# Performance work log

Hardware: AMD Instinct MI355X
Metric: run time of the kernel (lower is better)

The kernel has to match this reference:

```python
import jax, jax.numpy as jnp
import numpy as np

B, CH, CW, H, FH, FW = 32, 16, 16, 8, 4, 4
NQ = 64
NK = CH * FH * CW * FW  # 4096
D_IN, D_V, D_MODEL = 512, 64, 512


def setup_inputs() -> dict:
    key = jax.random.key(0)
    k1, k2, k3, k4, k5 = jax.random.split(key, 5)
    att12 = jax.random.uniform(k1, (B, CH, CW, H, FH, FW), dtype=jnp.float32)
    att3 = jax.random.uniform(k2, (B, H, NQ, CH * CW), dtype=jnp.float32)
    values = jax.random.normal(k3, (B, NK, D_IN), dtype=jnp.float32)
    # Learned params (xavier-ish scale)
    W_v = jax.random.normal(k4, (H * D_V, D_IN), dtype=jnp.float32) * (1.0 / np.sqrt(D_IN))
    b_v = jnp.zeros((H * D_V,), dtype=jnp.float32)
    W_o = jax.random.normal(k5, (D_MODEL, H * D_V), dtype=jnp.float32) * (1.0 / np.sqrt(H * D_V))
    b_o = jnp.zeros((D_MODEL,), dtype=jnp.float32)
    return {"att12": att12, "att3": att3, "values": values,
            "W_v": W_v, "b_v": b_v, "W_o": W_o, "b_o": b_o}


def reference(att12, att3, values, W_v, b_v, W_o, b_o):
    b_s, h, nq, _ = att3.shape
    ch = cw = CH
    fh, fw = att12.shape[-2:]
    nk = values.shape[1]
    d_v = W_v.shape[0] // h
    # v: [b, h, nk, d_v]
    v = (values @ W_v.T + b_v).reshape(b_s, nk, h, d_v).transpose(0, 2, 1, 3)
    # att12 -> [b, h, 1, ch, cw, fh, fw]
    a12 = jnp.transpose(att12, (0, 3, 1, 2, 4, 5))[:, :, None]
    # att3 -> [b, h, nq, ch, cw, 1, 1]
    a3 = att3.reshape(b_s, h, nq, ch, cw, 1, 1)
    # broadcast multiply, then interleave to key order (ch, fh, cw, fw)
    att = (a12 * a3).transpose(0, 1, 2, 3, 5, 4, 6).reshape(b_s, h, nq, nk)
    att = jax.nn.softmax(att, axis=-1)
    out = jnp.einsum('bhqk,bhkd->bhqd', att, v)
    out = out.transpose(0, 2, 1, 3).reshape(b_s, nq, h * d_v)
    return out @ W_o.T + b_o
```

## Files before the change

### kernel.cpp

```cpp
#include <hip/hip_runtime.h>

typedef short bf16x8 __attribute__((ext_vector_type(8)));
typedef short bf16x4 __attribute__((ext_vector_type(4)));
typedef float f32x4 __attribute__((ext_vector_type(4)));
typedef unsigned int u32x2 __attribute__((ext_vector_type(2)));
typedef unsigned int u32x4 __attribute__((ext_vector_type(4)));

__device__ __forceinline__ unsigned short f2bf(float f) {
  union { float f; unsigned u; } v; v.f = f;
  unsigned r = v.u + 0x7fffu + ((v.u >> 16) & 1u);
  return (unsigned short)(r >> 16);
}

__device__ __forceinline__ unsigned int pk2(float a, float b) {
  union { float f; unsigned u; } x, y; x.f = a; y.f = b;
  return __builtin_amdgcn_perm(y.u + 0x8000u, x.u + 0x8000u, 0x07060302u);
}

__device__ __forceinline__ void gld_lds16(const void* g, void* l) {
  __builtin_amdgcn_global_load_lds(
      (const __attribute__((address_space(1))) void*)g,
      (__attribute__((address_space(3))) void*)l, 16, 0, 0);
}

__global__ __launch_bounds__(256) void prep(const float* __restrict__ W_v,
                                            const float* __restrict__ W_o,
                                            const float* __restrict__ b_v,
                                            const float* __restrict__ b_o,
                                            unsigned short* __restrict__ Wvb,
                                            unsigned short* __restrict__ Wob,
                                            float* __restrict__ bias2) {
  int bid = blockIdx.x;
  if (bid < 512) {
    const float* in = (bid < 256) ? W_v : W_o;
    unsigned short* out = (bid < 256) ? Wvb : Wob;
    long i = (long)((bid & 255) * 256 + threadIdx.x) * 4;
    f32x4 d = *(const f32x4*)(in + i);
    u32x2 w; w[0] = pk2(d[0], d[1]); w[1] = pk2(d[2], d[3]);
    *(u32x2*)(out + i) = w;
  } else {
    int e = (bid - 512) * 256 + threadIdx.x;
    const float* wrow = W_o + (long)e * 512;
    float s = 0.f;
#pragma unroll 4
    for (int d = 0; d < 512; d += 4) {
      f32x4 w = *(const f32x4*)(wrow + d);
      f32x4 bv = *(const f32x4*)(b_v + d);
      s += w[0] * bv[0] + w[1] * bv[1] + w[2] * bv[2] + w[3] * bv[3];
    }
    bias2[e] = s + b_o[e];
  }
}

__global__ __launch_bounds__(256, 2) void vt_gemm(
    const unsigned short* __restrict__ Wvb, const float* __restrict__ V,
    unsigned short* __restrict__ vT) {
  const int t = threadIdx.x, lane = t & 63, wave = t >> 6;
  const int n0 = blockIdx.x * 128;
  const int m0 = blockIdx.y * 128;
  const int b = blockIdx.z;
  const float* Vb = V + (long)b * (4096L * 512) + (long)n0 * 512;

  __shared__ __align__(16) unsigned short As[3][128 * 32];
  __shared__ __align__(16) unsigned short Bs[2][128 * 32];

  const int wm = (wave >> 1) * 64, wn = (wave & 1) * 64;
  const int l16 = lane & 15, quad = lane >> 4;
  const int brow0 = t >> 3, bc4 = (t & 7) * 4;

  f32x4 breg[2][4];
  auto loadB = [&](int rr, int bank) {
    const int k0 = (rr < 16) ? rr * 32 : 0;
#pragma unroll
    for (int j = 0; j < 4; ++j)
      breg[bank][j] = *(const f32x4*)(Vb + (long)(brow0 + 32 * j) * 512 + k0 + bc4);
  };
  auto asyncA = [&](int rr, int slot) {
    const int k0 = (rr < 16) ? rr * 32 : 0;
#pragma unroll
    for (int s = 0; s < 2; ++s) {
      int li = s * 256 + t;
      int row = li >> 2, kq = (li & 3) * 8;
      gld_lds16(Wvb + (long)(m0 + row) * 512 + k0 + kq,
                (char*)&As[slot][0] + (s * 256 + wave * 64) * 16);
    }
  };

  f32x4 acc[4][4];
#pragma unroll
  for (int i = 0; i < 4; ++i)
#pragma unroll
    for (int j = 0; j < 4; ++j) acc[i][j] = (f32x4){0.f, 0.f, 0.f, 0.f};

  asyncA(0, 0);
  loadB(0, 0);
  asyncA(1, 1);
  loadB(1, 1);

  int slotR = 0, slotW = 2;
  for (int r = 0; r < 16; ++r) {
    const int bank = r & 1;
#pragma unroll
    for (int j = 0; j < 4; ++j) {
      u32x2 w;
      w[0] = pk2(breg[bank][j][0], breg[bank][j][1]);
      w[1] = pk2(breg[bank][j][2], breg[bank][j][3]);
      *(u32x2*)(&Bs[bank][(brow0 + 32 * j) * 32 + bc4]) = w;
    }
    loadB(r + 2, bank);
    asm volatile("s_waitcnt vmcnt(10) lgkmcnt(0)" ::: "memory");
    __builtin_amdgcn_s_barrier();
    asm volatile("" ::: "memory");
    asyncA(r + 2, slotW);
    asm volatile("" ::: "memory");
    bf16x8 af[4], bfv[4];
#pragma unroll
    for (int i = 0; i < 4; ++i)
      af[i] = *(const bf16x8*)(&As[slotR][(wm + i * 16 + l16) * 32 + quad * 8]);
#pragma unroll
    for (int j = 0; j < 4; ++j)
      bfv[j] = *(const bf16x8*)(&Bs[bank][(wn + j * 16 + l16) * 32 + quad * 8]);
#pragma unroll
    for (int i = 0; i < 4; ++i)
#pragma unroll
      for (int j = 0; j < 4; ++j)
        acc[i][j] = __builtin_amdgcn_mfma_f32_16x16x32_bf16(af[i], bfv[j], acc[i][j], 0, 0, 0);
    slotR = (slotR == 2) ? 0 : slotR + 1;
    slotW = (slotW == 2) ? 0 : slotW + 1;
  }
  asm volatile("s_waitcnt vmcnt(0)" ::: "memory");

  unsigned short* o = vT + (long)b * 2097152;
#pragma unroll
  for (int i = 0; i < 4; ++i)
#pragma unroll
    for (int j = 0; j < 4; ++j) {
      int col = n0 + wn + j * 16 + l16;
#pragma unroll
      for (int r = 0; r < 4; ++r) {
        int row = m0 + wm + i * 16 + quad * 4 + r;
        o[(long)row * 4096 + col] = f2bf(acc[i][j][r]);
      }
    }
}

__global__ __launch_bounds__(256, 2) void o_gemm(
    const float* __restrict__ att12, const float* __restrict__ att3,
    const unsigned short* __restrict__ vT, unsigned short* __restrict__ U) {
  const int bh = blockIdx.x;
  const int b = bh >> 3, h = bh & 7;
  const int t = threadIdx.x, lane = t & 63, wave = t >> 6;

  __shared__ __align__(16) unsigned short As[2][4 * 64 * 40];
  __shared__ __align__(16) unsigned short Bs[3][4 * 64 * 32];
  __shared__ float Ored[64 * 68];
  __shared__ float Zl[4][64];
  __shared__ float rZa[64];

  const unsigned short* vTb = vT + (long)b * 2097152 + (long)h * 64 * 4096;
  const int gq = t & 63, gw = t >> 6;
  const float* a3row = att3 + ((long)bh * 64 + gq) * 256;
  const float* a12b = att12 + (long)b * 32768 + h * 16;
  const int l16 = lane & 15, quad = lane >> 4;

  f32x4 acc[4][4];
#pragma unroll
  for (int i = 0; i < 4; ++i)
#pragma unroll
    for (int j = 0; j < 4; ++j) acc[i][j] = (f32x4){0.f, 0.f, 0.f, 0.f};
  float zacc = 0.f;

  unsigned int pk[16];
  auto genexp = [&](int r) {
    int kbase = gw * 1024 + r * 32;
    int ch = kbase >> 8, fh = (kbase >> 6) & 3, cw0 = (kbase >> 2) & 15;
    f32x4 y0 = *(const f32x4*)(a3row + ch * 16 + cw0);
    f32x4 y1 = *(const f32x4*)(a3row + ch * 16 + cw0 + 4);
    const float* ap = a12b + ch * 2048 + cw0 * 128 + fh * 4;
#pragma unroll
    for (int cw = 0; cw < 8; ++cw) {
      float y = (cw < 4) ? y0[cw] : y1[cw - 4];
      f32x4 x = *(const f32x4*)(ap + cw * 128);
      float e0 = __expf(x[0] * y), e1 = __expf(x[1] * y);
      float e2 = __expf(x[2] * y), e3 = __expf(x[3] * y);
      zacc += (e0 + e1) + (e2 + e3);
      pk[cw * 2] = pk2(e0, e1);
      pk[cw * 2 + 1] = pk2(e2, e3);
    }
  };
  auto asyncB = [&](int rr, int slot) {
    const int rc = (rr < 32) ? rr : 0;
#pragma unroll
    for (int s = 0; s < 4; ++s) {
      int row = t >> 2, kq = (t & 3) * 8;
      int kk = s * 1024 + rc * 32 + kq;
      gld_lds16(vTb + (long)row * 4096 + kk, (char*)&Bs[slot][0] + s * 4096 + wave * 1024);
    }
  };

  asyncB(0, 0);
  asyncB(1, 1);
  genexp(0);

  int slotR = 0, slotW = 2;
  for (int r = 0; r < 32; ++r) {
    const int abuf = r & 1;
    {
      unsigned short* dst = &As[abuf][gw * 2560 + gq * 40];
#pragma unroll
      for (int g = 0; g < 4; ++g)
        *(u32x4*)(dst + g * 8) = (u32x4){pk[g * 4], pk[g * 4 + 1], pk[g * 4 + 2], pk[g * 4 + 3]};
    }
    asm volatile("s_waitcnt vmcnt(4) lgkmcnt(0)" ::: "memory");
    __builtin_amdgcn_s_barrier();
    asm volatile("" ::: "memory");
    asyncB(r + 2, slotW);
    asm volatile("" ::: "memory");
    bf16x8 af[4], bfv[4];
#pragma unroll
    for (int i = 0; i < 4; ++i)
      af[i] = *(const bf16x8*)(&As[abuf][wave * 2560 + (i * 16 + l16) * 40 + quad * 8]);
#pragma unroll
    for (int j = 0; j < 4; ++j)
      bfv[j] = *(const bf16x8*)(&Bs[slotR][wave * 2048 + (j * 16 + l16) * 32 + quad * 8]);
#pragma unroll
    for (int i = 0; i < 4; ++i)
#pragma unroll
      for (int j = 0; j < 4; ++j)
        acc[i][j] = __builtin_amdgcn_mfma_f32_16x16x32_bf16(af[i], bfv[j], acc[i][j], 0, 0, 0);
    if (r < 31) genexp(r + 1);
    slotR = (slotR == 2) ? 0 : slotR + 1;
    slotW = (slotW == 2) ? 0 : slotW + 1;
  }
  asm volatile("s_waitcnt vmcnt(0)" ::: "memory");

  Zl[gw][gq] = zacc;
  __syncthreads();
  if (t < 64) rZa[t] = 1.0f / (Zl[0][t] + Zl[1][t] + Zl[2][t] + Zl[3][t]);
#pragma unroll
  for (int w = 0; w < 4; ++w) {
    if (wave == w) {
#pragma unroll
      for (int i = 0; i < 4; ++i)
#pragma unroll
        for (int j = 0; j < 4; ++j) {
          int col = j * 16 + l16;
#pragma unroll
          for (int rr = 0; rr < 4; ++rr) {
            int row = i * 16 + quad * 4 + rr;
            if (w == 0) Ored[row * 68 + col] = acc[i][j][rr];
            else Ored[row * 68 + col] += acc[i][j][rr];
          }
        }
    }
    __syncthreads();
  }
  {
    int q = t >> 2, dv0 = (t & 3) * 16;
    float rz = rZa[q];
    unsigned short* up = U + ((long)(b * 64 + q)) * 512 + h * 64 + dv0;
    u32x4 o0, o1;
#pragma unroll
    for (int j = 0; j < 4; ++j)
      o0[j] = pk2(Ored[q * 68 + dv0 + 2 * j] * rz, Ored[q * 68 + dv0 + 2 * j + 1] * rz);
#pragma unroll
    for (int j = 0; j < 4; ++j)
      o1[j] = pk2(Ored[q * 68 + dv0 + 8 + 2 * j] * rz, Ored[q * 68 + dv0 + 9 + 2 * j] * rz);
    *(u32x4*)(up) = o0;
    *(u32x4*)(up + 8) = o1;
  }
}

template <int BM, int BN>
__global__ __launch_bounds__(256, 2) void gemm_bt(
    const unsigned short* __restrict__ A, const unsigned short* __restrict__ Bt,
    float* __restrict__ C, const float* __restrict__ bias,
    int K, int lda, int ldb, int ldc) {
  constexpr int BK = 32;
  const int t = threadIdx.x;
  const int lane = t & 63;
  const int wave = t >> 6;
  const int m0 = blockIdx.y * BM;
  const int n0 = blockIdx.x * BN;

  A += (long)m0 * lda;
  Bt += (long)n0 * ldb;

  __shared__ __align__(16) unsigned short As[3][BM * BK];
  __shared__ __align__(16) unsigned short Bs[3][BN * BK];

  constexpr int TM = BM / 32;
  constexpr int TN = BN / 32;
  const int wm = (wave >> 1) * (BM / 2);
  const int wn = (wave & 1) * (BN / 2);
  const int l16 = lane & 15;
  const int quad = lane >> 4;

  f32x4 acc[TM][TN];
#pragma unroll
  for (int i = 0; i < TM; ++i)
#pragma unroll
    for (int j = 0; j < TN; ++j) acc[i][j] = (f32x4){0.f, 0.f, 0.f, 0.f};

  constexpr int ASHOT = (BM * 4) / 256;
  constexpr int BSHOT = (BN * 4) / 256;
  const int NIT = K / BK;

  auto stage = [&](int rr, int slot) {
    const int k0 = ((rr < NIT) ? rr : 0) * BK;
#pragma unroll
    for (int s = 0; s < ASHOT; ++s) {
      int li = s * 256 + t;
      int row = li >> 2, kq = (li & 3) * 8;
      gld_lds16(A + (long)row * lda + k0 + kq,
                (char*)&As[slot][0] + (s * 256 + wave * 64) * 16);
    }
#pragma unroll
    for (int s = 0; s < BSHOT; ++s) {
      int li = s * 256 + t;
      int row = li >> 2, kq = (li & 3) * 8;
      gld_lds16(Bt + (long)row * ldb + k0 + kq,
                (char*)&Bs[slot][0] + (s * 256 + wave * 64) * 16);
    }
  };

  stage(0, 0);
  stage(1, 1);

  int slotR = 0, slotW = 2;
  for (int r = 0; r < NIT; ++r) {
    asm volatile("s_waitcnt vmcnt(2)" ::: "memory");
    __builtin_amdgcn_s_barrier();
    asm volatile("" ::: "memory");
    stage(r + 2, slotW);
    asm volatile("" ::: "memory");
    bf16x8 af[TM], bfv[TN];
#pragma unroll
    for (int i = 0; i < TM; ++i)
      af[i] = *(const bf16x8*)(&As[slotR][(wm + i * 16 + l16) * BK + quad * 8]);
#pragma unroll
    for (int j = 0; j < TN; ++j)
      bfv[j] = *(const bf16x8*)(&Bs[slotR][(wn + j * 16 + l16) * BK + quad * 8]);
#pragma unroll
    for (int i = 0; i < TM; ++i)
#pragma unroll
      for (int j = 0; j < TN; ++j)
        acc[i][j] = __builtin_amdgcn_mfma_f32_16x16x32_bf16(af[i], bfv[j], acc[i][j], 0, 0, 0);
    slotR = (slotR == 2) ? 0 : slotR + 1;
    slotW = (slotW == 2) ? 0 : slotW + 1;
  }
  asm volatile("s_waitcnt vmcnt(0)" ::: "memory");

#pragma unroll
  for (int i = 0; i < TM; ++i) {
#pragma unroll
    for (int j = 0; j < TN; ++j) {
      int col = wn + j * 16 + l16;
#pragma unroll
      for (int r = 0; r < 4; ++r) {
        int row = wm + i * 16 + quad * 4 + r;
        C[(long)(m0 + row) * ldc + (n0 + col)] = acc[i][j][r] + bias[n0 + col];
      }
    }
  }
}

extern "C" void kernel_launch(void* const* d_in, const int* in_sizes, int n_in,
                              void* d_out, int out_size, void* d_ws, size_t ws_size,
                              hipStream_t stream) {
  const float* att12 = (const float*)d_in[0];
  const float* att3  = (const float*)d_in[1];
  const float* values = (const float*)d_in[2];
  const float* W_v = (const float*)d_in[3];
  const float* b_v = (const float*)d_in[4];
  const float* W_o = (const float*)d_in[5];
  const float* b_o = (const float*)d_in[6];
  float* out = (float*)d_out;

  char* ws = (char*)d_ws;
  unsigned short* vT    = (unsigned short*)(ws);
  unsigned short* U     = (unsigned short*)(ws + 134217728L);
  unsigned short* Wvb   = (unsigned short*)(ws + 136314880L);
  unsigned short* Wob   = (unsigned short*)(ws + 136839168L);
  float*          bias2 = (float*)(ws + 137363456L);

  prep<<<dim3(514), dim3(256), 0, stream>>>(W_v, W_o, b_v, b_o, Wvb, Wob, bias2);

  vt_gemm<<<dim3(32, 4, 32), dim3(256), 0, stream>>>(Wvb, values, vT);

  o_gemm<<<dim3(256), dim3(256), 0, stream>>>(att12, att3, vT, U);

  gemm_bt<64, 64><<<dim3(8, 32), dim3(256), 0, stream>>>(
      U, Wob, out, bias2, 512, 512, 512, 512);

  (void)in_sizes; (void)n_in; (void)out_size; (void)ws_size;
}
```

Measured before the change: 557.2 us.

## Enlarge vt_gemm M tile to 256 and simplify to double-buffered pipeline

Doubles the per-block M tile of the value-projection GEMM so each fp32 values tile is read by half as many blocks, reducing global traffic on the largest input. The prefetch scheme is simplified from a three-slot A ring with two-deep B register prefetch to a plain double buffer with a block barrier. This raises accumulator register use and shortens the prefetch distance, which may expose more memory latency or lower occupancy.

```diff
diff --git a/kernel.cpp b/kernel.cpp
--- a/kernel.cpp
+++ b/kernel.cpp
@@ -57,82 +57,72 @@
     unsigned short* __restrict__ vT) {
   const int t = threadIdx.x, lane = t & 63, wave = t >> 6;
   const int n0 = blockIdx.x * 128;
-  const int m0 = blockIdx.y * 128;
+  const int m0 = blockIdx.y * 256;
   const int b = blockIdx.z;
   const float* Vb = V + (long)b * (4096L * 512) + (long)n0 * 512;
 
-  __shared__ __align__(16) unsigned short As[3][128 * 32];
+  __shared__ __align__(16) unsigned short As[2][256 * 32];
   __shared__ __align__(16) unsigned short Bs[2][128 * 32];
 
-  const int wm = (wave >> 1) * 64, wn = (wave & 1) * 64;
+  const int wm = (wave >> 1) * 128, wn = (wave & 1) * 64;
   const int l16 = lane & 15, quad = lane >> 4;
   const int brow0 = t >> 3, bc4 = (t & 7) * 4;
 
-  f32x4 breg[2][4];
-  auto loadB = [&](int rr, int bank) {
-    const int k0 = (rr < 16) ? rr * 32 : 0;
-#pragma unroll
-    for (int j = 0; j < 4; ++j)
-      breg[bank][j] = *(const f32x4*)(Vb + (long)(brow0 + 32 * j) * 512 + k0 + bc4);
-  };
-  auto asyncA = [&](int rr, int slot) {
-    const int k0 = (rr < 16) ? rr * 32 : 0;
-#pragma unroll
-    for (int s = 0; s < 2; ++s) {
+  f32x4 breg[4];
+  auto loadB = [&](int k0) {
+#pragma unroll
+    for (int j = 0; j < 4; ++j)
+      breg[j] = *(const f32x4*)(Vb + (long)(brow0 + 32 * j) * 512 + k0 + bc4);
+  };
+  auto asyncA = [&](int k0, int buf) {
+#pragma unroll
+    for (int s = 0; s < 4; ++s) {
       int li = s * 256 + t;
       int row = li >> 2, kq = (li & 3) * 8;
       gld_lds16(Wvb + (long)(m0 + row) * 512 + k0 + kq,
-                (char*)&As[slot][0] + (s * 256 + wave * 64) * 16);
-    }
-  };
-
-  f32x4 acc[4][4];
-#pragma unroll
-  for (int i = 0; i < 4; ++i)
+                (char*)&As[buf][0] + (s * 256 + wave * 64) * 16);
+    }
+  };
+
+  f32x4 acc[8][4];
+#pragma unroll
+  for (int i = 0; i < 8; ++i)
 #pragma unroll
     for (int j = 0; j < 4; ++j) acc[i][j] = (f32x4){0.f, 0.f, 0.f, 0.f};
 
   asyncA(0, 0);
-  loadB(0, 0);
-  asyncA(1, 1);
-  loadB(1, 1);
-
-  int slotR = 0, slotW = 2;
+  loadB(0);
+
   for (int r = 0; r < 16; ++r) {
-    const int bank = r & 1;
+    const int buf = r & 1;
 #pragma unroll
     for (int j = 0; j < 4; ++j) {
       u32x2 w;
-      w[0] = pk2(breg[bank][j][0], breg[bank][j][1]);
-      w[1] = pk2(breg[bank][j][2], breg[bank][j][3]);
-      *(u32x2*)(&Bs[bank][(brow0 + 32 * j) * 32 + bc4]) = w;
-    }
-    loadB(r + 2, bank);
-    asm volatile("s_waitcnt vmcnt(10) lgkmcnt(0)" ::: "memory");
-    __builtin_amdgcn_s_barrier();
-    asm volatile("" ::: "memory");
-    asyncA(r + 2, slotW);
-    asm volatile("" ::: "memory");
-    bf16x8 af[4], bfv[4];
-#pragma unroll
-    for (int i = 0; i < 4; ++i)
-      af[i] = *(const bf16x8*)(&As[slotR][(wm + i * 16 + l16) * 32 + quad * 8]);
-#pragma unroll
-    for (int j = 0; j < 4; ++j)
-      bfv[j] = *(const bf16x8*)(&Bs[bank][(wn + j * 16 + l16) * 32 + quad * 8]);
-#pragma unroll
-    for (int i = 0; i < 4; ++i)
+      w[0] = pk2(breg[j][0], breg[j][1]);
+      w[1] = pk2(breg[j][2], breg[j][3]);
+      *(u32x2*)(&Bs[buf][(brow0 + 32 * j) * 32 + bc4]) = w;
+    }
+    __syncthreads();
+    if (r < 15) {
+      loadB((r + 1) * 32);
+      asyncA((r + 1) * 32, buf ^ 1);
+    }
+    bf16x8 bfv[4];
+#pragma unroll
+    for (int j = 0; j < 4; ++j)
+      bfv[j] = *(const bf16x8*)(&Bs[buf][(wn + j * 16 + l16) * 32 + quad * 8]);
+#pragma unroll
+    for (int i = 0; i < 8; ++i) {
+      bf16x8 af = *(const bf16x8*)(&As[buf][(wm + i * 16 + l16) * 32 + quad * 8]);
 #pragma unroll
       for (int j = 0; j < 4; ++j)
-        acc[i][j] = __builtin_amdgcn_mfma_f32_16x16x32_bf16(af[i], bfv[j], acc[i][j], 0, 0, 0);
-    slotR = (slotR == 2) ? 0 : slotR + 1;
-    slotW = (slotW == 2) ? 0 : slotW + 1;
-  }
-  asm volatile("s_waitcnt vmcnt(0)" ::: "memory");
+        acc[i][j] = __builtin_amdgcn_mfma_f32_16x16x32_bf16(af, bfv[j], acc[i][j], 0, 0, 0);
+    }
+  }
 
   unsigned short* o = vT + (long)b * 2097152;
 #pragma unroll
-  for (int i = 0; i < 4; ++i)
+  for (int i = 0; i < 8; ++i)
 #pragma unroll
     for (int j = 0; j < 4; ++j) {
       int col = n0 + wn + j * 16 + l16;
@@ -386,7 +376,7 @@
 
   prep<<<dim3(514), dim3(256), 0, stream>>>(W_v, W_o, b_v, b_o, Wvb, Wob, bias2);
 
-  vt_gemm<<<dim3(32, 4, 32), dim3(256), 0, stream>>>(Wvb, values, vT);
+  vt_gemm<<<dim3(32, 2, 32), dim3(256), 0, stream>>>(Wvb, values, vT);
 
   o_gemm<<<dim3(256), dim3(256), 0, stream>>>(att12, att3, vT, U);
 
```

Measured after the change: 531.2 us. -4.7%, faster.
